# Performance work log

Measured on AMD Instinct MI355X. Metric: run time of the kernel, lower is better.

Reference implementation:

```python
import jax, jax.numpy as jnp
import numpy as np

N, D = 1024, 256  # number of matrices (power of 2), matrix dim
EPS = 0.002       # near-identity noise scale to keep 1024-long product stable


def setup_inputs() -> dict:
    key = jax.random.key(0)
    k1, k2 = jax.random.split(key)
    x = jax.random.normal(k1, (1, D), dtype=jnp.float32)
    m = jnp.eye(D, dtype=jnp.float32)[None] + EPS * jax.random.normal(
        k2, (N, D, D), dtype=jnp.float32)
    return {"x": x, "m": m}


def reference(x, m):
    # The torch module performs a Blelloch up-sweep (pairwise bmm) building
    # per-level products, then a down-sweep producing the exclusive prefix
    # applications of x: res[k] = x @ (m_0 @ ... @ m_{k-1}) for k = 0..N.
    # lax.associative_scan with matmul is the idiomatic log-depth tree scan
    # computing the same math: P[k] = m_0 @ ... @ m_k (inclusive, in order).
    P = jax.lax.associative_scan(jnp.matmul, m)      # [N, D, D]
    applied = jnp.matmul(x, P)[:, 0, :]              # [N, D]: x @ P[k]
    # res[0] = x (empty prefix), res[1..N] = x @ P[0..N-1]
    res = jnp.concatenate([x, applied], axis=0)      # [N+1, D]
    return res
```

## Files before the change

### kernel.cpp

```cpp
#include <hip/hip_runtime.h>


#define D 256
#define DD 65536

typedef __attribute__((ext_vector_type(8))) short short8;
typedef __attribute__((ext_vector_type(4))) float f4;

__device__ __forceinline__ float bf2f(unsigned short u) {
  return __uint_as_float(((unsigned)u) << 16);
}
__device__ __forceinline__ unsigned short f2bf(float f) {
  unsigned u = __float_as_uint(f);
  u += 0x7FFFu + ((u >> 16) & 1u);
  return (unsigned short)(u >> 16);
}
#define LSWZ(i15, lq) (((((i15) & 15)) + ((lq) << 4)) ^ (lq))

__global__ __launch_bounds__(256) void gemm_mfma(
    const float* __restrict__ aF, const unsigned short* __restrict__ aBf,
    long aMul, long aOff,
    const float* __restrict__ bF, const unsigned short* __restrict__ bBf,
    long bMul, long bOff,
    unsigned short* __restrict__ out)
{
  __shared__ __attribute__((aligned(16))) unsigned short As[32768];
  unsigned short* Bs = As + 16384;

  const int  bx  = blockIdx.x;
  const int  nmb = ((int)gridDim.x) >> 4;
  const int  xcd = bx & 7, q = bx >> 3;
  const long mat = (long)(xcd * (nmb >> 3)) + (q >> 4);
  const int  tile = q & 15;
  const int  m0 = (tile >> 2) << 6, n0 = (tile & 3) << 6;
  const long aBase = (mat * aMul + aOff) * (long)DD;
  const long bBase = (mat * bMul + bOff) * (long)DD;
  const int t = threadIdx.x;
  const int w = t >> 6, l = t & 63, lm = l & 15, lq4 = l >> 4;
  const int lswz = l ^ lq4;

  if (aF) {
#pragma unroll
    for (int p = 0; p < 16; ++p) {
      const int idx = (p << 10) + (t << 2);
      const int r = idx >> 8, k = idx & 255;
      const int gi = m0 + r;
      float4 v = *(const float4*)(aF + aBase + (long)gi * D + k);
      v.x -= (gi == k + 0) ? 1.f : 0.f;
      v.y -= (gi == k + 1) ? 1.f : 0.f;
      v.z -= (gi == k + 2) ? 1.f : 0.f;
      v.w -= (gi == k + 3) ? 1.f : 0.f;
      const int lq = (k >> 3) & 3;
      const int slot = (((r >> 4) << 3) + (k >> 5)) * 64 + LSWZ(r, lq);
      ushort4 o = { f2bf(v.x), f2bf(v.y), f2bf(v.z), f2bf(v.w) };
      *(ushort4*)&As[(slot << 3) + (k & 7)] = o;
    }
  } else {
#pragma unroll
    for (int p = 0; p < 8; ++p) {
      const int sidx = (p << 11) + (t << 3);
      const int r = sidx >> 8, k = sidx & 255;
      const uint4 v = *(const uint4*)(aBf + aBase + (long)(m0 + r) * D + k);
      const int lq = (k >> 3) & 3;
      const int slot = (((r >> 4) << 3) + (k >> 5)) * 64 + LSWZ(r, lq);
      *(uint4*)&As[slot << 3] = v;
    }
  }
  {
    const int n4 = (t & 15) << 2;
    const int kb0 = (t >> 4) << 3;
#pragma unroll
    for (int kp = 0; kp < 2; ++kp) {
      const int k8 = kb0 + (kp << 7);
      __attribute__((aligned(16))) unsigned short tmp[4][8];
      if (bF) {
#pragma unroll
        for (int kk = 0; kk < 8; ++kk) {
          const int gk = k8 + kk, gn = n0 + n4;
          float4 v = *(const float4*)(bF + bBase + (long)gk * D + gn);
          v.x -= (gk == gn + 0) ? 1.f : 0.f;
          v.y -= (gk == gn + 1) ? 1.f : 0.f;
          v.z -= (gk == gn + 2) ? 1.f : 0.f;
          v.w -= (gk == gn + 3) ? 1.f : 0.f;
          tmp[0][kk] = f2bf(v.x); tmp[1][kk] = f2bf(v.y);
          tmp[2][kk] = f2bf(v.z); tmp[3][kk] = f2bf(v.w);
        }
      } else {
#pragma unroll
        for (int kk = 0; kk < 8; ++kk) {
          const ushort4 v = *(const ushort4*)(bBf + bBase + (long)(k8 + kk) * D + n0 + n4);
          tmp[0][kk] = v.x; tmp[1][kk] = v.y; tmp[2][kk] = v.z; tmp[3][kk] = v.w;
        }
      }
      const int lq = (k8 >> 3) & 3, kt = k8 >> 5;
#pragma unroll
      for (int jj = 0; jj < 4; ++jj) {
        const int n = n4 + jj;
        const int slot = (((n >> 4) << 3) + kt) * 64 + LSWZ(n, lq);
        *(uint4*)&Bs[slot << 3] = *(const uint4*)&tmp[jj][0];
      }
    }
  }
  __syncthreads();

  f4 acc[4] = {{0.f,0.f,0.f,0.f},{0.f,0.f,0.f,0.f},
               {0.f,0.f,0.f,0.f},{0.f,0.f,0.f,0.f}};
#pragma unroll
  for (int kt = 0; kt < 8; ++kt) {
    const short8 a = *(const short8*)&As[((((w << 3) + kt) << 6) + lswz) << 3];
#pragma unroll
    for (int f = 0; f < 4; ++f) {
      const short8 b = *(const short8*)&Bs[((((f << 3) + kt) << 6) + lswz) << 3];
      acc[f] = __builtin_amdgcn_mfma_f32_16x16x32_bf16(a, b, acc[f], 0, 0, 0);
    }
  }

  float sv[4][4];
#pragma unroll
  for (int f = 0; f < 4; ++f) {
    const int gj_l = (f << 4) + lm;
    const int gj   = n0 + gj_l;
    const int lqA  = (gj >> 3) & 3;
#pragma unroll
    for (int r = 0; r < 4; ++r) {
      const int gi_l = (w << 4) + (lq4 << 2) + r;
      const int giG  = m0 + gi_l;
      const int slotA = (((gi_l >> 4) << 3) + (gj >> 5)) * 64 + LSWZ(gi_l, lqA);
      const float da = bf2f(As[(slotA << 3) + (gj & 7)]);
      const int lqB  = (giG >> 3) & 3;
      const int slotB = (((gj_l >> 4) << 3) + (giG >> 5)) * 64 + LSWZ(gj_l, lqB);
      const float db = bf2f(Bs[(slotB << 3) + (giG & 7)]);
      sv[f][r] = acc[f][r] + da + db;
    }
  }
  __syncthreads();

  unsigned short* Cs = As;
#pragma unroll
  for (int f = 0; f < 4; ++f)
#pragma unroll
    for (int r = 0; r < 4; ++r)
      Cs[((w << 4) + (lq4 << 2) + r) * 66 + (f << 4) + lm] = f2bf(sv[f][r]);
  __syncthreads();
  {
    const int row = t >> 2, c0 = (t & 3) << 4;
    const unsigned int* Cw = (const unsigned int*)Cs;
    const int wb = row * 33 + ((t & 3) << 3);
    unsigned int wbuf[8];
#pragma unroll
    for (int i = 0; i < 8; ++i) wbuf[i] = Cw[wb + i];
    unsigned short* og = out + mat * (long)DD + (long)(m0 + row) * D + n0 + c0;
    uint4 o0 = { wbuf[0], wbuf[1], wbuf[2], wbuf[3] };
    uint4 o1 = { wbuf[4], wbuf[5], wbuf[6], wbuf[7] };
    *(uint4*)og = o0;
    *((uint4*)og + 1) = o1;
  }
}

__global__ __launch_bounds__(1024) void scan_top8(
    const float* __restrict__ x, const unsigned short* __restrict__ S,
    float* __restrict__ w8)
{
  __shared__ float v[D];
  __shared__ float ps[4][D];
  const int t = threadIdx.x, col = t & 255, kq = t >> 8;
  if (t < D) v[t] = x[t];
  __syncthreads();
  for (int g = 0; g < 8; ++g) {
    if (t < D) w8[g * D + t] = v[t];
    const unsigned short* M = S + (long)g * DD + (long)(kq * 64) * D + col;
    float acc = 0.f;
#pragma unroll 8
    for (int i = 0; i < 64; ++i)
      acc += v[kq * 64 + i] * bf2f(M[(long)i * D]);
    ps[kq][col] = acc;
    __syncthreads();
    if (t < D) v[t] += ps[0][t] + ps[1][t] + ps[2][t] + ps[3][t];
    __syncthreads();
  }
}

__global__ __launch_bounds__(1024) void descend(
    const float* __restrict__ src, const unsigned short* __restrict__ mats,
    float* __restrict__ dst)
{
  __shared__ float v[D];
  __shared__ float ps[4][D];
  const int g = blockIdx.x, t = threadIdx.x, col = t & 255, kq = t >> 8;
  if (t < D) v[t] = src[(long)g * D + t];
  __syncthreads();
  if (t < D) dst[(long)(2 * g) * D + t] = v[t];
  const unsigned short* M = mats + (long)(2 * g) * DD + (long)(kq * 64) * D + col;
  float acc = 0.f;
#pragma unroll 8
  for (int i = 0; i < 64; ++i)
    acc += v[kq * 64 + i] * bf2f(M[(long)i * D]);
  ps[kq][col] = acc;
  __syncthreads();
  if (t < D)
    dst[(long)(2 * g + 1) * D + t] = v[t] + ps[0][t] + ps[1][t] + ps[2][t] + ps[3][t];
}

__global__ __launch_bounds__(1024) void bottom(
    const float* __restrict__ u, const float* __restrict__ m,
    float* __restrict__ out)
{
  __shared__ float v[D];
  __shared__ float ps[4][D];
  const int c = blockIdx.x, t = threadIdx.x, col = t & 255, kq = t >> 8;
  if (t < D) v[t] = u[(long)c * D + t];
  __syncthreads();
  if (t < D) out[(long)(4 * c) * D + t] = v[t];
  const int steps = (c == 255) ? 4 : 3;
  for (int s = 0; s < steps; ++s) {
    const float* M = m + (long)(4 * c + s) * DD + (long)(kq * 64) * D + col;
    float acc = 0.f;
#pragma unroll 8
    for (int i = 0; i < 64; ++i)
      acc += v[kq * 64 + i] * M[(long)i * D];
    ps[kq][col] = acc;
    __syncthreads();
    if (t < D) {
      float s2 = ps[0][t] + ps[1][t] + ps[2][t] + ps[3][t];
      v[t] = s2;
      out[(long)(4 * c + s + 1) * D + t] = s2;
    }
    __syncthreads();
  }
}

__global__ __launch_bounds__(256) void fallback_seq(
    const float* __restrict__ x, const float* __restrict__ m,
    float* __restrict__ out)
{
  __shared__ float v[D];
  const int t = threadIdx.x;
  v[t] = x[t];
  __syncthreads();
  for (int k = 0; k < 1024; ++k) {
    out[(long)k * D + t] = v[t];
    const float* M = m + (long)k * DD;
    float acc = 0.f;
    for (int i = 0; i < D; ++i) acc += v[i] * M[(long)i * D + t];
    __syncthreads();
    v[t] = acc;
    __syncthreads();
  }
  out[(long)1024 * D + t] = v[t];
}

extern "C" void kernel_launch(void* const* d_in, const int* in_sizes, int n_in,
                              void* d_out, int out_size, void* d_ws, size_t ws_size,
                              hipStream_t stream) {
  const float* x = (const float*)d_in[0];
  const float* m = (const float*)d_in[1];
  float* out = (float*)d_out;

  const size_t NEED = 67624960;
  if (ws_size < NEED) {
    fallback_seq<<<1, 256, 0, stream>>>(x, m, out);
    return;
  }

  char* w8 = (char*)d_ws;
  unsigned short* buf0 = (unsigned short*)(w8);
  unsigned short* Qb   = (unsigned short*)(w8 + 33554432);
  unsigned short* Q2   = (unsigned short*)(w8);
  unsigned short* Q4   = (unsigned short*)(w8 + 16777216);
  unsigned short* Rm   = (unsigned short*)(w8 + 25165824);
  unsigned short* S64  = (unsigned short*)(w8 + 29360128);
  unsigned short* S128 = (unsigned short*)(w8 + 31457280);
  float* wv  = (float*)(w8 + 67108864);
  float* w8v = wv;
  float* w16 = wv + 2048;
  float* w32 = wv + 6144;
  float* u4  = wv + 14336;
  float* u2  = wv + 30720;
  float* uu  = wv + 63488;

  const dim3 blk(256), vblk(1024);
  gemm_mfma<<<dim3(4096), blk, 0, stream>>>(m, nullptr, 2, 0, m, nullptr, 2, 1, buf0);
  gemm_mfma<<<dim3(2048), blk, 0, stream>>>(nullptr, buf0, 2, 0, nullptr, buf0, 2, 1, Qb);
  gemm_mfma<<<dim3(4096), blk, 0, stream>>>(m + 512L * DD, nullptr, 2, 0,
                                            m + 512L * DD, nullptr, 2, 1, buf0);
  gemm_mfma<<<dim3(2048), blk, 0, stream>>>(nullptr, buf0, 2, 0, nullptr, buf0, 2, 1,
                                            Qb + 128L * DD);
  gemm_mfma<<<dim3(2048), blk, 0, stream>>>(nullptr, Qb, 2, 0, nullptr, Qb, 2, 1, Q2);
  gemm_mfma<<<dim3(1024), blk, 0, stream>>>(nullptr, Q2, 2, 0, nullptr, Q2, 2, 1, Q4);
  gemm_mfma<<<dim3(512),  blk, 0, stream>>>(nullptr, Q4, 2, 0, nullptr, Q4, 2, 1, Rm);
  gemm_mfma<<<dim3(256),  blk, 0, stream>>>(nullptr, Rm, 2, 0, nullptr, Rm, 2, 1, S64);
  gemm_mfma<<<dim3(128),  blk, 0, stream>>>(nullptr, S64, 2, 0, nullptr, S64, 2, 1, S128);
  scan_top8<<<dim3(1), vblk, 0, stream>>>(x, S128, w8v);
  descend<<<dim3(8),   vblk, 0, stream>>>(w8v, S64, w16);
  descend<<<dim3(16),  vblk, 0, stream>>>(w16, Rm,  w32);
  descend<<<dim3(32),  vblk, 0, stream>>>(w32, Q4,  u4);
  descend<<<dim3(64),  vblk, 0, stream>>>(u4,  Q2,  u2);
  descend<<<dim3(128), vblk, 0, stream>>>(u2,  Qb,  uu);
  bottom<<<dim3(256), vblk, 0, stream>>>(uu, m, out);
}
```

Baseline: 576.6 us.

## Keep A operand in registers, fuse descent kernels into one tail kernel

The GEMM kernel now loads each wave's A fragment directly from global memory into registers. This halves shared memory use so launch bounds can request four blocks per CU, and it uses packed bf16 conversion intrinsics. The scan_top8, descend and bottom kernels are replaced by a single tail kernel in which each block rebuilds its prefix vector from x by walking the power-of-two product levels. That removes six dependent launches but repeats vector-matrix work across blocks. With a larger workspace, the first level runs as one 8192-block launch instead of being split in halves.

```diff
diff --git a/kernel.cpp b/kernel.cpp
--- a/kernel.cpp
+++ b/kernel.cpp
@@ -1,4 +1,5 @@
 #include <hip/hip_runtime.h>
+#include <hip/hip_bf16.h>
 
 
 #define D 256
@@ -11,21 +12,27 @@
   return __uint_as_float(((unsigned)u) << 16);
 }
 __device__ __forceinline__ unsigned short f2bf(float f) {
-  unsigned u = __float_as_uint(f);
-  u += 0x7FFFu + ((u >> 16) & 1u);
-  return (unsigned short)(u >> 16);
+  __hip_bfloat16 h = __float2bfloat16(f);
+  unsigned short u;
+  __builtin_memcpy(&u, &h, 2);
+  return u;
+}
+__device__ __forceinline__ unsigned f2bf2(float lo, float hi) {
+  __hip_bfloat162 h = __float22bfloat162_rn(make_float2(lo, hi));
+  unsigned u;
+  __builtin_memcpy(&u, &h, 4);
+  return u;
 }
 #define LSWZ(i15, lq) (((((i15) & 15)) + ((lq) << 4)) ^ (lq))
 
-__global__ __launch_bounds__(256) void gemm_mfma(
+__global__ __launch_bounds__(256, 4) void gemm_mfma(
     const float* __restrict__ aF, const unsigned short* __restrict__ aBf,
     long aMul, long aOff,
     const float* __restrict__ bF, const unsigned short* __restrict__ bBf,
     long bMul, long bOff,
     unsigned short* __restrict__ out)
 {
-  __shared__ __attribute__((aligned(16))) unsigned short As[32768];
-  unsigned short* Bs = As + 16384;
+  __shared__ __attribute__((aligned(16))) unsigned short Bs[16384];
 
   const int  bx  = blockIdx.x;
   const int  nmb = ((int)gridDim.x) >> 4;
@@ -39,65 +46,80 @@
   const int w = t >> 6, l = t & 63, lm = l & 15, lq4 = l >> 4;
   const int lswz = l ^ lq4;
 
+  const int R = m0 + (w << 4) + lm;
+  short8 areg[8];
   if (aF) {
-#pragma unroll
-    for (int p = 0; p < 16; ++p) {
-      const int idx = (p << 10) + (t << 2);
-      const int r = idx >> 8, k = idx & 255;
-      const int gi = m0 + r;
-      float4 v = *(const float4*)(aF + aBase + (long)gi * D + k);
-      v.x -= (gi == k + 0) ? 1.f : 0.f;
-      v.y -= (gi == k + 1) ? 1.f : 0.f;
-      v.z -= (gi == k + 2) ? 1.f : 0.f;
-      v.w -= (gi == k + 3) ? 1.f : 0.f;
-      const int lq = (k >> 3) & 3;
-      const int slot = (((r >> 4) << 3) + (k >> 5)) * 64 + LSWZ(r, lq);
-      ushort4 o = { f2bf(v.x), f2bf(v.y), f2bf(v.z), f2bf(v.w) };
-      *(ushort4*)&As[(slot << 3) + (k & 7)] = o;
+    const float* ap = aF + aBase + (long)R * D + (lq4 << 3);
+#pragma unroll
+    for (int kt = 0; kt < 8; ++kt) {
+      const int k0 = (kt << 5) + (lq4 << 3);
+      const float4 v0 = *(const float4*)(ap + (kt << 5));
+      const float4 v1 = *(const float4*)(ap + (kt << 5) + 4);
+      union { short8 v8; unsigned u[4]; } ou;
+      ou.u[0] = f2bf2(v0.x - ((R == k0 + 0) ? 1.f : 0.f),
+                      v0.y - ((R == k0 + 1) ? 1.f : 0.f));
+      ou.u[1] = f2bf2(v0.z - ((R == k0 + 2) ? 1.f : 0.f),
+                      v0.w - ((R == k0 + 3) ? 1.f : 0.f));
+      ou.u[2] = f2bf2(v1.x - ((R == k0 + 4) ? 1.f : 0.f),
+                      v1.y - ((R == k0 + 5) ? 1.f : 0.f));
+      ou.u[3] = f2bf2(v1.z - ((R == k0 + 6) ? 1.f : 0.f),
+                      v1.w - ((R == k0 + 7) ? 1.f : 0.f));
+      areg[kt] = ou.v8;
     }
   } else {
-#pragma unroll
-    for (int p = 0; p < 8; ++p) {
-      const int sidx = (p << 11) + (t << 3);
-      const int r = sidx >> 8, k = sidx & 255;
-      const uint4 v = *(const uint4*)(aBf + aBase + (long)(m0 + r) * D + k);
-      const int lq = (k >> 3) & 3;
-      const int slot = (((r >> 4) << 3) + (k >> 5)) * 64 + LSWZ(r, lq);
-      *(uint4*)&As[slot << 3] = v;
-    }
-  }
+    const unsigned short* ap = aBf + aBase + (long)R * D + (lq4 << 3);
+#pragma unroll
+    for (int kt = 0; kt < 8; ++kt)
+      areg[kt] = *(const short8*)(ap + (kt << 5));
+  }
+
   {
     const int n4 = (t & 15) << 2;
     const int kb0 = (t >> 4) << 3;
 #pragma unroll
     for (int kp = 0; kp < 2; ++kp) {
       const int k8 = kb0 + (kp << 7);
-      __attribute__((aligned(16))) unsigned short tmp[4][8];
+      const int lq = (k8 >> 3) & 3, kt = k8 >> 5;
       if (bF) {
-#pragma unroll
-        for (int kk = 0; kk < 8; ++kk) {
-          const int gk = k8 + kk, gn = n0 + n4;
-          float4 v = *(const float4*)(bF + bBase + (long)gk * D + gn);
-          v.x -= (gk == gn + 0) ? 1.f : 0.f;
-          v.y -= (gk == gn + 1) ? 1.f : 0.f;
-          v.z -= (gk == gn + 2) ? 1.f : 0.f;
-          v.w -= (gk == gn + 3) ? 1.f : 0.f;
-          tmp[0][kk] = f2bf(v.x); tmp[1][kk] = f2bf(v.y);
-          tmp[2][kk] = f2bf(v.z); tmp[3][kk] = f2bf(v.w);
+        unsigned tmpu[4][4];
+#pragma unroll
+        for (int kk = 0; kk < 8; kk += 2) {
+          const int gka = k8 + kk, gkb = gka + 1, gn = n0 + n4;
+          float4 va = *(const float4*)(bF + bBase + (long)gka * D + gn);
+          float4 vb = *(const float4*)(bF + bBase + (long)gkb * D + gn);
+          va.x -= (gka == gn + 0) ? 1.f : 0.f;
+          va.y -= (gka == gn + 1) ? 1.f : 0.f;
+          va.z -= (gka == gn + 2) ? 1.f : 0.f;
+          va.w -= (gka == gn + 3) ? 1.f : 0.f;
+          vb.x -= (gkb == gn + 0) ? 1.f : 0.f;
+          vb.y -= (gkb == gn + 1) ? 1.f : 0.f;
+          vb.z -= (gkb == gn + 2) ? 1.f : 0.f;
+          vb.w -= (gkb == gn + 3) ? 1.f : 0.f;
+          tmpu[0][kk >> 1] = f2bf2(va.x, vb.x);
+          tmpu[1][kk >> 1] = f2bf2(va.y, vb.y);
+          tmpu[2][kk >> 1] = f2bf2(va.z, vb.z);
+          tmpu[3][kk >> 1] = f2bf2(va.w, vb.w);
+        }
+#pragma unroll
+        for (int jj = 0; jj < 4; ++jj) {
+          const int n = n4 + jj;
+          const int slot = (((n >> 4) << 3) + kt) * 64 + LSWZ(n, lq);
+          uint4 st = { tmpu[jj][0], tmpu[jj][1], tmpu[jj][2], tmpu[jj][3] };
+          *(uint4*)&Bs[slot << 3] = st;
         }
       } else {
+        __attribute__((aligned(16))) unsigned short tmp[4][8];
 #pragma unroll
         for (int kk = 0; kk < 8; ++kk) {
           const ushort4 v = *(const ushort4*)(bBf + bBase + (long)(k8 + kk) * D + n0 + n4);
           tmp[0][kk] = v.x; tmp[1][kk] = v.y; tmp[2][kk] = v.z; tmp[3][kk] = v.w;
         }
-      }
-      const int lq = (k8 >> 3) & 3, kt = k8 >> 5;
-#pragma unroll
-      for (int jj = 0; jj < 4; ++jj) {
-        const int n = n4 + jj;
-        const int slot = (((n >> 4) << 3) + kt) * 64 + LSWZ(n, lq);
-        *(uint4*)&Bs[slot << 3] = *(const uint4*)&tmp[jj][0];
+#pragma unroll
+        for (int jj = 0; jj < 4; ++jj) {
+          const int n = n4 + jj;
+          const int slot = (((n >> 4) << 3) + kt) * 64 + LSWZ(n, lq);
+          *(uint4*)&Bs[slot << 3] = *(const uint4*)&tmp[jj][0];
+        }
       }
     }
   }
@@ -107,49 +129,49 @@
                {0.f,0.f,0.f,0.f},{0.f,0.f,0.f,0.f}};
 #pragma unroll
   for (int kt = 0; kt < 8; ++kt) {
-    const short8 a = *(const short8*)&As[((((w << 3) + kt) << 6) + lswz) << 3];
 #pragma unroll
     for (int f = 0; f < 4; ++f) {
       const short8 b = *(const short8*)&Bs[((((f << 3) + kt) << 6) + lswz) << 3];
-      acc[f] = __builtin_amdgcn_mfma_f32_16x16x32_bf16(a, b, acc[f], 0, 0, 0);
-    }
-  }
-
-  float sv[4][4];
+      acc[f] = __builtin_amdgcn_mfma_f32_16x16x32_bf16(areg[kt], b, acc[f], 0, 0, 0);
+    }
+  }
+
 #pragma unroll
   for (int f = 0; f < 4; ++f) {
     const int gj_l = (f << 4) + lm;
     const int gj   = n0 + gj_l;
-    const int lqA  = (gj >> 3) & 3;
 #pragma unroll
     for (int r = 0; r < 4; ++r) {
       const int gi_l = (w << 4) + (lq4 << 2) + r;
       const int giG  = m0 + gi_l;
-      const int slotA = (((gi_l >> 4) << 3) + (gj >> 5)) * 64 + LSWZ(gi_l, lqA);
-      const float da = bf2f(As[(slotA << 3) + (gj & 7)]);
+      float da;
+      if (aF)
+        da = aF[aBase + (long)giG * D + gj] - ((giG == gj) ? 1.f : 0.f);
+      else
+        da = bf2f(aBf[aBase + (long)giG * D + gj]);
       const int lqB  = (giG >> 3) & 3;
       const int slotB = (((gj_l >> 4) << 3) + (giG >> 5)) * 64 + LSWZ(gj_l, lqB);
       const float db = bf2f(Bs[(slotB << 3) + (giG & 7)]);
-      sv[f][r] = acc[f][r] + da + db;
-    }
-  }
-  __syncthreads();
-
-  unsigned short* Cs = As;
+      acc[f][r] += da + db;
+    }
+  }
+  __syncthreads();
+
+  unsigned short* Cs = Bs;
 #pragma unroll
   for (int f = 0; f < 4; ++f)
 #pragma unroll
     for (int r = 0; r < 4; ++r)
-      Cs[((w << 4) + (lq4 << 2) + r) * 66 + (f << 4) + lm] = f2bf(sv[f][r]);
+      Cs[((w << 4) + (lq4 << 2) + r) * 66 + (f << 4) + lm] = f2bf(acc[f][r]);
   __syncthreads();
   {
-    const int row = t >> 2, c0 = (t & 3) << 4;
+    const int row = t >> 2, c0g = (t & 3) << 4;
     const unsigned int* Cw = (const unsigned int*)Cs;
     const int wb = row * 33 + ((t & 3) << 3);
     unsigned int wbuf[8];
 #pragma unroll
     for (int i = 0; i < 8; ++i) wbuf[i] = Cw[wb + i];
-    unsigned short* og = out + mat * (long)DD + (long)(m0 + row) * D + n0 + c0;
+    unsigned short* og = out + mat * (long)DD + (long)(m0 + row) * D + n0 + c0g;
     uint4 o0 = { wbuf[0], wbuf[1], wbuf[2], wbuf[3] };
     uint4 o1 = { wbuf[4], wbuf[5], wbuf[6], wbuf[7] };
     *(uint4*)og = o0;
@@ -157,63 +179,48 @@
   }
 }
 
-__global__ __launch_bounds__(1024) void scan_top8(
-    const float* __restrict__ x, const unsigned short* __restrict__ S,
-    float* __restrict__ w8)
-{
-  __shared__ float v[D];
-  __shared__ float ps[4][D];
-  const int t = threadIdx.x, col = t & 255, kq = t >> 8;
-  if (t < D) v[t] = x[t];
-  __syncthreads();
-  for (int g = 0; g < 8; ++g) {
-    if (t < D) w8[g * D + t] = v[t];
-    const unsigned short* M = S + (long)g * DD + (long)(kq * 64) * D + col;
-    float acc = 0.f;
-#pragma unroll 8
-    for (int i = 0; i < 64; ++i)
-      acc += v[kq * 64 + i] * bf2f(M[(long)i * D]);
-    ps[kq][col] = acc;
-    __syncthreads();
-    if (t < D) v[t] += ps[0][t] + ps[1][t] + ps[2][t] + ps[3][t];
-    __syncthreads();
-  }
-}
-
-__global__ __launch_bounds__(1024) void descend(
-    const float* __restrict__ src, const unsigned short* __restrict__ mats,
-    float* __restrict__ dst)
-{
-  __shared__ float v[D];
-  __shared__ float ps[4][D];
-  const int g = blockIdx.x, t = threadIdx.x, col = t & 255, kq = t >> 8;
-  if (t < D) v[t] = src[(long)g * D + t];
-  __syncthreads();
-  if (t < D) dst[(long)(2 * g) * D + t] = v[t];
-  const unsigned short* M = mats + (long)(2 * g) * DD + (long)(kq * 64) * D + col;
+__device__ __forceinline__ void apply_bf16(const unsigned short* __restrict__ Mb,
+                                           float* v, float (*ps)[D],
+                                           int t, int col, int kq) {
+  const unsigned short* M = Mb + (long)(kq * 64) * D + col;
   float acc = 0.f;
 #pragma unroll 8
   for (int i = 0; i < 64; ++i)
     acc += v[kq * 64 + i] * bf2f(M[(long)i * D]);
   ps[kq][col] = acc;
   __syncthreads();
-  if (t < D)
-    dst[(long)(2 * g + 1) * D + t] = v[t] + ps[0][t] + ps[1][t] + ps[2][t] + ps[3][t];
-}
-
-__global__ __launch_bounds__(1024) void bottom(
-    const float* __restrict__ u, const float* __restrict__ m,
-    float* __restrict__ out)
+  if (t < D) v[t] += ps[0][t] + ps[1][t] + ps[2][t] + ps[3][t];
+  __syncthreads();
+}
+
+__global__ __launch_bounds__(1024) void tail_fused(
+    const float* __restrict__ x,
+    const unsigned short* __restrict__ sp128, const unsigned short* __restrict__ sp64,
+    const unsigned short* __restrict__ sp32,  const unsigned short* __restrict__ sp16,
+    const unsigned short* __restrict__ sp8,   const unsigned short* __restrict__ sp4,
+    const float* __restrict__ m, float* __restrict__ out)
 {
   __shared__ float v[D];
   __shared__ float ps[4][D];
   const int c = blockIdx.x, t = threadIdx.x, col = t & 255, kq = t >> 8;
-  if (t < D) v[t] = u[(long)c * D + t];
-  __syncthreads();
-  if (t < D) out[(long)(4 * c) * D + t] = v[t];
+  if (t < D) v[t] = x[t];
+  __syncthreads();
+  const int L = c << 2;
+
+  int pos = 0;
+#pragma unroll 1
+  while (pos + 128 <= L) { apply_bf16(sp128 + (long)(pos >> 7) * DD, v, ps, t, col, kq); pos += 128; }
+  if (pos + 64 <= L) { apply_bf16(sp64 + (long)(pos >> 6) * DD, v, ps, t, col, kq); pos += 64; }
+  if (pos + 32 <= L) { apply_bf16(sp32 + (long)(pos >> 5) * DD, v, ps, t, col, kq); pos += 32; }
+  if (pos + 16 <= L) { apply_bf16(sp16 + (long)(pos >> 4) * DD, v, ps, t, col, kq); pos += 16; }
+  if (pos + 8 <= L)  { apply_bf16(sp8  + (long)(pos >> 3) * DD, v, ps, t, col, kq); pos += 8; }
+  if (pos + 4 <= L)  { apply_bf16(sp4  + (long)(pos >> 2) * DD, v, ps, t, col, kq); pos += 4; }
+
+  if (t < D) out[(long)L * D + t] = v[t];
   const int steps = (c == 255) ? 4 : 3;
+#pragma unroll 1
   for (int s = 0; s < steps; ++s) {
-    const float* M = m + (long)(4 * c + s) * DD + (long)(kq * 64) * D + col;
+    const float* M = m + (long)(L + s) * DD + (long)(kq * 64) * D + col;
     float acc = 0.f;
 #pragma unroll 8
     for (int i = 0; i < 64; ++i)
@@ -221,9 +228,9 @@
     ps[kq][col] = acc;
     __syncthreads();
     if (t < D) {
-      float s2 = ps[0][t] + ps[1][t] + ps[2][t] + ps[3][t];
+      const float s2 = ps[0][t] + ps[1][t] + ps[2][t] + ps[3][t];
       v[t] = s2;
-      out[(long)(4 * c + s + 1) * D + t] = s2;
+      out[(long)(L + s + 1) * D + t] = s2;
     }
     __syncthreads();
   }
@@ -256,45 +263,47 @@
   const float* m = (const float*)d_in[1];
   float* out = (float*)d_out;
 
-  const size_t NEED = 67624960;
-  if (ws_size < NEED) {
-    fallback_seq<<<1, 256, 0, stream>>>(x, m, out);
-    return;
-  }
-
   char* w8 = (char*)d_ws;
-  unsigned short* buf0 = (unsigned short*)(w8);
-  unsigned short* Qb   = (unsigned short*)(w8 + 33554432);
-  unsigned short* Q2   = (unsigned short*)(w8);
-  unsigned short* Q4   = (unsigned short*)(w8 + 16777216);
-  unsigned short* Rm   = (unsigned short*)(w8 + 25165824);
-  unsigned short* S64  = (unsigned short*)(w8 + 29360128);
-  unsigned short* S128 = (unsigned short*)(w8 + 31457280);
-  float* wv  = (float*)(w8 + 67108864);
-  float* w8v = wv;
-  float* w16 = wv + 2048;
-  float* w32 = wv + 6144;
-  float* u4  = wv + 14336;
-  float* u2  = wv + 30720;
-  float* uu  = wv + 63488;
-
+  const size_t MB = 1048576;
   const dim3 blk(256), vblk(1024);
-  gemm_mfma<<<dim3(4096), blk, 0, stream>>>(m, nullptr, 2, 0, m, nullptr, 2, 1, buf0);
-  gemm_mfma<<<dim3(2048), blk, 0, stream>>>(nullptr, buf0, 2, 0, nullptr, buf0, 2, 1, Qb);
-  gemm_mfma<<<dim3(4096), blk, 0, stream>>>(m + 512L * DD, nullptr, 2, 0,
-                                            m + 512L * DD, nullptr, 2, 1, buf0);
-  gemm_mfma<<<dim3(2048), blk, 0, stream>>>(nullptr, buf0, 2, 0, nullptr, buf0, 2, 1,
-                                            Qb + 128L * DD);
-  gemm_mfma<<<dim3(2048), blk, 0, stream>>>(nullptr, Qb, 2, 0, nullptr, Qb, 2, 1, Q2);
-  gemm_mfma<<<dim3(1024), blk, 0, stream>>>(nullptr, Q2, 2, 0, nullptr, Q2, 2, 1, Q4);
-  gemm_mfma<<<dim3(512),  blk, 0, stream>>>(nullptr, Q4, 2, 0, nullptr, Q4, 2, 1, Rm);
-  gemm_mfma<<<dim3(256),  blk, 0, stream>>>(nullptr, Rm, 2, 0, nullptr, Rm, 2, 1, S64);
-  gemm_mfma<<<dim3(128),  blk, 0, stream>>>(nullptr, S64, 2, 0, nullptr, S64, 2, 1, S128);
-  scan_top8<<<dim3(1), vblk, 0, stream>>>(x, S128, w8v);
-  descend<<<dim3(8),   vblk, 0, stream>>>(w8v, S64, w16);
-  descend<<<dim3(16),  vblk, 0, stream>>>(w16, Rm,  w32);
-  descend<<<dim3(32),  vblk, 0, stream>>>(w32, Q4,  u4);
-  descend<<<dim3(64),  vblk, 0, stream>>>(u4,  Q2,  u2);
-  descend<<<dim3(128), vblk, 0, stream>>>(u2,  Qb,  uu);
-  bottom<<<dim3(256), vblk, 0, stream>>>(uu, m, out);
-}
+
+  if (ws_size >= 127 * MB) {
+    unsigned short* T2   = (unsigned short*)(w8);
+    unsigned short* Qb   = (unsigned short*)(w8 + 64 * MB);
+    unsigned short* Q2   = (unsigned short*)(w8 + 96 * MB);
+    unsigned short* Q4   = (unsigned short*)(w8 + 112 * MB);
+    unsigned short* Rm   = (unsigned short*)(w8 + 120 * MB);
+    unsigned short* S64  = (unsigned short*)(w8 + 124 * MB);
+    unsigned short* S128 = (unsigned short*)(w8 + 126 * MB);
+    gemm_mfma<<<dim3(8192), blk, 0, stream>>>(m, nullptr, 2, 0, m, nullptr, 2, 1, T2);
+    gemm_mfma<<<dim3(4096), blk, 0, stream>>>(nullptr, T2, 2, 0, nullptr, T2, 2, 1, Qb);
+    gemm_mfma<<<dim3(2048), blk, 0, stream>>>(nullptr, Qb, 2, 0, nullptr, Qb, 2, 1, Q2);
+    gemm_mfma<<<dim3(1024), blk, 0, stream>>>(nullptr, Q2, 2, 0, nullptr, Q2, 2, 1, Q4);
+    gemm_mfma<<<dim3(512),  blk, 0, stream>>>(nullptr, Q4, 2, 0, nullptr, Q4, 2, 1, Rm);
+    gemm_mfma<<<dim3(256),  blk, 0, stream>>>(nullptr, Rm, 2, 0, nullptr, Rm, 2, 1, S64);
+    gemm_mfma<<<dim3(128),  blk, 0, stream>>>(nullptr, S64, 2, 0, nullptr, S64, 2, 1, S128);
+    tail_fused<<<dim3(256), vblk, 0, stream>>>(x, S128, S64, Rm, Q4, Q2, Qb, m, out);
+  } else if (ws_size >= 67108864) {
+    unsigned short* buf0 = (unsigned short*)(w8);
+    unsigned short* Qb   = (unsigned short*)(w8 + 33554432);
+    unsigned short* Q2   = (unsigned short*)(w8);
+    unsigned short* Q4   = (unsigned short*)(w8 + 16777216);
+    unsigned short* Rm   = (unsigned short*)(w8 + 25165824);
+    unsigned short* S64  = (unsigned short*)(w8 + 29360128);
+    unsigned short* S128 = (unsigned short*)(w8 + 31457280);
+    gemm_mfma<<<dim3(4096), blk, 0, stream>>>(m, nullptr, 2, 0, m, nullptr, 2, 1, buf0);
+    gemm_mfma<<<dim3(2048), blk, 0, stream>>>(nullptr, buf0, 2, 0, nullptr, buf0, 2, 1, Qb);
+    gemm_mfma<<<dim3(4096), blk, 0, stream>>>(m + 512L * DD, nullptr, 2, 0,
+                                              m + 512L * DD, nullptr, 2, 1, buf0);
+    gemm_mfma<<<dim3(2048), blk, 0, stream>>>(nullptr, buf0, 2, 0, nullptr, buf0, 2, 1,
+                                              Qb + 128L * DD);
+    gemm_mfma<<<dim3(2048), blk, 0, stream>>>(nullptr, Qb, 2, 0, nullptr, Qb, 2, 1, Q2);
+    gemm_mfma<<<dim3(1024), blk, 0, stream>>>(nullptr, Q2, 2, 0, nullptr, Q2, 2, 1, Q4);
+    gemm_mfma<<<dim3(512),  blk, 0, stream>>>(nullptr, Q4, 2, 0, nullptr, Q4, 2, 1, Rm);
+    gemm_mfma<<<dim3(256),  blk, 0, stream>>>(nullptr, Rm, 2, 0, nullptr, Rm, 2, 1, S64);
+    gemm_mfma<<<dim3(128),  blk, 0, stream>>>(nullptr, S64, 2, 0, nullptr, S64, 2, 1, S128);
+    tail_fused<<<dim3(256), vblk, 0, stream>>>(x, S128, S64, Rm, Q4, Q2, Qb, m, out);
+  } else {
+    fallback_seq<<<dim3(1), blk, 0, stream>>>(x, m, out);
+  }
+}
```

After: 573.2 us. Within noise of the previous version (-0.6%).
